# Kernel tuning notes

Measured on AMD Instinct MI355X. Metric: run time of the kernel, lower is better.

The kernel has to match this reference:

```python
import jax, jax.numpy as jnp
import numpy as np

N_NODES = 50000
IN_CH = 128
HID = 128
N_EDGES = 800000


def _glorot(key, shape):
    fan_in, fan_out = shape[0], shape[1]
    lim = (6.0 / (fan_in + fan_out)) ** 0.5
    return jax.random.uniform(key, shape, jnp.float32, -lim, lim)


def setup_inputs() -> dict:
    key = jax.random.key(0)
    ks = jax.random.split(key, 8)
    x = jax.random.normal(ks[0], (N_NODES, IN_CH), jnp.float32)
    edge_index = jax.random.randint(ks[1], (2, N_EDGES), 0, N_NODES, jnp.int64)
    return {
        "x": x,
        "edge_index": edge_index,
        # SAGEConv1: lin_l (with bias) applied to mean-aggregated neighbors,
        # lin_r (no bias) applied to root features (PyG defaults, mean aggr)
        "W1l": _glorot(ks[2], (IN_CH, HID)),
        "b1l": jnp.zeros((HID,), jnp.float32),
        "W1r": _glorot(ks[3], (IN_CH, HID)),
        # SAGEConv2
        "W2l": _glorot(ks[4], (HID, HID)),
        "b2l": jnp.zeros((HID,), jnp.float32),
        "W2r": _glorot(ks[5], (HID, HID)),
        # final Linear(hidden, 1)
        "Wout": _glorot(ks[6], (HID, 1)),
        "bout": jnp.zeros((1,), jnp.float32),
    }


def _sage_conv(x, src, dst, Wl, bl, Wr, n_nodes):
    # gather source features along edges, mean-reduce into destinations
    msgs = x[src]                                                # [E, D]
    sums = jax.ops.segment_sum(msgs, dst, num_segments=n_nodes)  # [N, D]
    cnt = jax.ops.segment_sum(jnp.ones((src.shape[0], 1), x.dtype), dst,
                              num_segments=n_nodes)              # [N, 1]
    agg = sums / jnp.maximum(cnt, 1.0)
    return agg @ Wl + bl + x @ Wr


def reference(x, edge_index, W1l, b1l, W1r, W2l, b2l, W2r, Wout, bout):
    src, dst = edge_index[0], edge_index[1]
    n = x.shape[0]
    h = jax.nn.relu(_sage_conv(x, src, dst, W1l, b1l, W1r, n))
    h = jax.nn.relu(_sage_conv(h, src, dst, W2l, b2l, W2r, n))
    return (h @ Wout + bout).squeeze(-1)  # [N]
```

## Files before the change

### kernel.cpp

```cpp
#include <hip/hip_runtime.h>

#define D 128
#define LSTR 132

typedef __attribute__((ext_vector_type(8))) short short8;
typedef __attribute__((ext_vector_type(4))) float f32x4;

static __device__ __forceinline__ unsigned short f2bf(float f) {
    unsigned u = __float_as_uint(f);
    return (unsigned short)((u + 0x7fffu + ((u >> 16) & 1u)) >> 16);
}
static __device__ __forceinline__ float b2f(unsigned short u) {
    return __uint_as_float(((unsigned)u) << 16);
}


__global__ void prep_kernel(const float* __restrict__ x,
                            const float* __restrict__ W1l,
                            const float* __restrict__ W1r,
                            const float* __restrict__ W2l,
                            const float* __restrict__ W2r,
                            unsigned* __restrict__ xb2,
                            unsigned short* __restrict__ Bt1,
                            unsigned short* __restrict__ Bt2,
                            int* __restrict__ cnt, int NX2, int Ncnt) {
    const int i = blockIdx.x * blockDim.x + threadIdx.x;
    if (i < NX2) {
        const float2 v = *(const float2*)(x + 2 * (size_t)i);
        xb2[i] = (unsigned)f2bf(v.x) | ((unsigned)f2bf(v.y) << 16);
    } else if (i < NX2 + 2 * 32768) {
        const int j = i - NX2;
        const int which = j >> 15;
        const int jj = j & 32767;
        const int n = jj >> 8;
        const int k = jj & 255;
        const float* Wl = which ? W2l : W1l;
        const float* Wr = which ? W2r : W1r;
        const float w = (k < 128) ? Wl[k * 128 + n] : Wr[(k - 128) * 128 + n];
        (which ? Bt2 : Bt1)[jj] = f2bf(w);
    } else if (i < NX2 + 2 * 32768 + Ncnt) {
        cnt[i - NX2 - 2 * 32768] = 0;
    }
}

__global__ void hist_kernel(const int* __restrict__ dst, int E,
                            int* __restrict__ cnt) {
    int i = blockIdx.x * blockDim.x + threadIdx.x;
    if (i < E) atomicAdd(&cnt[dst[i]], 1);
}

__global__ __launch_bounds__(256) void alloc_kernel(
    const int* __restrict__ cnt, int* __restrict__ cursor,
    int* __restrict__ blk_range, int* __restrict__ gctr, int nchunks) {
    const int c = blockIdx.x * 8 + (threadIdx.x >> 5);
    const int l = threadIdx.x & 31;
    if (c >= nchunks) return;
    const int r0 = c * 32;
    const int v = cnt[r0 + l];
    int s = v;
#pragma unroll
    for (int off = 1; off < 32; off <<= 1) {
        const int u = __shfl_up(s, off, 32);
        if (l >= off) s += u;
    }
    const int tot = __shfl(s, 31, 32);
    int base = 0;
    if (l == 0) base = atomicAdd(gctr, tot);
    base = __shfl(base, 0, 32);
    cursor[r0 + l] = base + s - v;
    if (l == 0) {
        blk_range[2 * c] = base;
        blk_range[2 * c + 1] = base + tot;
    }
}

__global__ void fill_kernel(const int* __restrict__ src,
                            const int* __restrict__ dst, int E,
                            int* __restrict__ cursor,
                            unsigned* __restrict__ csr) {
    int e = blockIdx.x * blockDim.x + threadIdx.x;
    if (e < E) {
        int d = dst[e];
        int p = atomicAdd(&cursor[d], 1);
        csr[p] = (unsigned)src[e] | ((unsigned)d << 16);
    }
}

template <bool HEAD>
__global__ __launch_bounds__(256) void sage_kernel(
    const unsigned short* __restrict__ xb, const unsigned* __restrict__ csr,
    const int* __restrict__ cnt, const int* __restrict__ blk_range,
    const unsigned short* __restrict__ Bt,
    const float* __restrict__ bl, const float* __restrict__ Wout,
    const float* __restrict__ bout, unsigned short* __restrict__ hb_out,
    float* __restrict__ out, int N) {
    __shared__ float aggL[32 * LSTR];
    __shared__ float invL[32];
    __shared__ float redH[32 * 2];

    const int b = blockIdx.x;
    const int i0 = b * 32;
    const int t = threadIdx.x;
    const int g = t >> 5;
    const int l = t & 31;
    const int c4 = l << 2;

    for (int i = t; i < 32 * LSTR; i += 256) aggL[i] = 0.f;
    if (t < 32) invL[t] = 1.0f / fmaxf((float)cnt[i0 + t], 1.0f);
    __syncthreads();

    const int rs0 = blk_range[2 * b];
    const int re0 = blk_range[2 * b + 1];
    const int nE = re0 - rs0;
    int e = rs0 + ((nE * g) >> 3);
    const int ee = rs0 + ((nE * (g + 1)) >> 3);

    float4 acc = make_float4(0.f, 0.f, 0.f, 0.f);
    int cur = (e < ee) ? (int)(csr[e] >> 16) - i0 : -1;

    auto load4 = [&](unsigned p) -> float4 {
        const ushort4 u =
            *(const ushort4*)(xb + (size_t)(p & 0xffffu) * D + c4);
        float4 v;
        v.x = b2f(u.x); v.y = b2f(u.y); v.z = b2f(u.z); v.w = b2f(u.w);
        return v;
    };
    auto step = [&](unsigned p, const float4& v) {
        const int r = (int)(p >> 16) - i0;
        if (r != cur) {
            float* q = aggL + cur * LSTR + c4;
            atomicAdd(q + 0, acc.x);
            atomicAdd(q + 1, acc.y);
            atomicAdd(q + 2, acc.z);
            atomicAdd(q + 3, acc.w);
            acc = make_float4(0.f, 0.f, 0.f, 0.f);
            cur = r;
        }
        acc.x += v.x; acc.y += v.y; acc.z += v.z; acc.w += v.w;
    };

    while (e + 8 <= ee) {
        const unsigned p0 = csr[e + 0], p1 = csr[e + 1];
        const unsigned p2 = csr[e + 2], p3 = csr[e + 3];
        const unsigned p4 = csr[e + 4], p5 = csr[e + 5];
        const unsigned p6 = csr[e + 6], p7 = csr[e + 7];
        const float4 v0 = load4(p0), v1 = load4(p1), v2 = load4(p2),
                     v3 = load4(p3), v4 = load4(p4), v5 = load4(p5),
                     v6 = load4(p6), v7 = load4(p7);
        step(p0, v0); step(p1, v1); step(p2, v2); step(p3, v3);
        step(p4, v4); step(p5, v5); step(p6, v6); step(p7, v7);
        e += 8;
    }
    while (e < ee) {
        const unsigned p = csr[e];
        step(p, load4(p));
        ++e;
    }
    if (cur >= 0) {
        float* q = aggL + cur * LSTR + c4;
        atomicAdd(q + 0, acc.x);
        atomicAdd(q + 1, acc.y);
        atomicAdd(q + 2, acc.z);
        atomicAdd(q + 3, acc.w);
    }
    __syncthreads();

    const int wave = t >> 6;
    const int lane = t & 63;
    const int ln = lane & 15;
    const int quad = lane >> 4;
    const int mtile = wave & 1;
    const int nt0 = (wave >> 1) * 4;
    const int mrow = mtile * 16 + ln;
    const int gmr = i0 + mrow;
    const float inv = invL[mrow];

    f32x4 acc4[4] = {f32x4{0.f, 0.f, 0.f, 0.f}, f32x4{0.f, 0.f, 0.f, 0.f},
                     f32x4{0.f, 0.f, 0.f, 0.f}, f32x4{0.f, 0.f, 0.f, 0.f}};

#pragma unroll
    for (int s = 0; s < 4; ++s) {
        const int kb = s * 32 + quad * 8;
        const float* ap = aggL + mrow * LSTR + kb;
        const float4 fa = *(const float4*)ap;
        const float4 fb = *(const float4*)(ap + 4);
        const short8 aA = {(short)f2bf(fa.x * inv), (short)f2bf(fa.y * inv),
                           (short)f2bf(fa.z * inv), (short)f2bf(fa.w * inv),
                           (short)f2bf(fb.x * inv), (short)f2bf(fb.y * inv),
                           (short)f2bf(fb.z * inv), (short)f2bf(fb.w * inv)};
        short8 aX = {0, 0, 0, 0, 0, 0, 0, 0};
        if (gmr < N) aX = *(const short8*)(xb + (size_t)gmr * D + kb);
#pragma unroll
        for (int nt = 0; nt < 4; ++nt) {
            const int n = (nt0 + nt) * 16 + ln;
            const short8 b1 = *(const short8*)(Bt + n * 256 + kb);
            const short8 b2 = *(const short8*)(Bt + n * 256 + 128 + kb);
            acc4[nt] = __builtin_amdgcn_mfma_f32_16x16x32_bf16(aA, b1, acc4[nt],
                                                               0, 0, 0);
            acc4[nt] = __builtin_amdgcn_mfma_f32_16x16x32_bf16(aX, b2, acc4[nt],
                                                               0, 0, 0);
        }
    }

    float biasv[4], woutv[4];
#pragma unroll
    for (int nt = 0; nt < 4; ++nt) {
        const int col = (nt0 + nt) * 16 + ln;
        biasv[nt] = bl[col];
        if (HEAD) woutv[nt] = Wout[col];
    }

    if (!HEAD) {
#pragma unroll
        for (int r = 0; r < 4; ++r) {
            const int gr = i0 + mtile * 16 + quad * 4 + r;
            if (gr < N) {
#pragma unroll
                for (int nt = 0; nt < 4; ++nt) {
                    const int col = (nt0 + nt) * 16 + ln;
                    const float v = fmaxf(acc4[nt][r] + biasv[nt], 0.f);
                    hb_out[(size_t)gr * D + col] = f2bf(v);
                }
            }
        }
    } else {
        const float b0 = bout[0];
#pragma unroll
        for (int r = 0; r < 4; ++r) {
            const int row = mtile * 16 + quad * 4 + r;
            float p = 0.f;
#pragma unroll
            for (int nt = 0; nt < 4; ++nt) {
                const float v = fmaxf(acc4[nt][r] + biasv[nt], 0.f);
                p += v * woutv[nt];
            }
            p += __shfl_xor(p, 1);
            p += __shfl_xor(p, 2);
            p += __shfl_xor(p, 4);
            p += __shfl_xor(p, 8);
            if (ln == 0) redH[row * 2 + (wave >> 1)] = p;
        }
        __syncthreads();
        if (t < 32) {
            const int gr = i0 + t;
            if (gr < N) out[gr] = redH[t * 2] + redH[t * 2 + 1] + b0;
        }
    }
}

extern "C" void kernel_launch(void* const* d_in, const int* in_sizes, int n_in,
                              void* d_out, int out_size, void* d_ws,
                              size_t ws_size, hipStream_t stream) {
    const float* x = (const float*)d_in[0];
    const int* ei = (const int*)d_in[1];
    const float* W1l = (const float*)d_in[2];
    const float* b1l = (const float*)d_in[3];
    const float* W1r = (const float*)d_in[4];
    const float* W2l = (const float*)d_in[5];
    const float* b2l = (const float*)d_in[6];
    const float* W2r = (const float*)d_in[7];
    const float* Wout = (const float*)d_in[8];
    const float* bout = (const float*)d_in[9];

    const int N = in_sizes[0] / D;
    const int E = in_sizes[1] / 2;
    const int* src = ei;
    const int* dst = ei + E;

    const size_t Npad = (size_t)((N + 66 + 255) & ~255);
    const size_t Epad = (size_t)((E + 255) & ~255);
    int* cnt = (int*)d_ws;
    int* gctr = cnt + Npad - 1;
    int* cursor = cnt + Npad;
    int* blk_range = cursor + Npad;
    unsigned* csr = (unsigned*)(blk_range + 4096);
    unsigned short* xb = (unsigned short*)(csr + Epad);
    unsigned short* hb = xb + (size_t)N * D;
    unsigned short* Bt1 = hb + (size_t)N * D;
    unsigned short* Bt2 = Bt1 + 128 * 256;
    float* out = (float*)d_out;

    const int nchunks = (N + 31) / 32;
    const int NX2 = N * D / 2;
    const int prep_total = NX2 + 2 * 32768 + (int)Npad;

    prep_kernel<<<(prep_total + 255) / 256, 256, 0, stream>>>(
        x, W1l, W1r, W2l, W2r, (unsigned*)xb, Bt1, Bt2, cnt, NX2, (int)Npad);
    hist_kernel<<<(E + 255) / 256, 256, 0, stream>>>(dst, E, cnt);
    alloc_kernel<<<(nchunks + 7) / 8, 256, 0, stream>>>(cnt, cursor, blk_range,
                                                        gctr, nchunks);
    fill_kernel<<<(E + 255) / 256, 256, 0, stream>>>(src, dst, E, cursor, csr);

    sage_kernel<false><<<nchunks, 256, 0, stream>>>(
        xb, csr, cnt, blk_range, Bt1, b1l, nullptr, nullptr, hb, nullptr, N);
    sage_kernel<true><<<nchunks, 256, 0, stream>>>(
        hb, csr, cnt, blk_range, Bt2, b2l, Wout, bout, nullptr, out, N);
}
```

Baseline: 313.9 us.

## Replace global-atomic CSR build with block-local tile binning and in-kernel row sort

Replaces the global histogram/alloc/fill CSR construction, which relies on per-node global atomics, with a two-level scheme. Edges are binned per 32-node tile using shared-memory histograms, a per-bin column scan and a single-block prefix scan, then scattered into tile-grouped order. Each sage kernel then counts rows and sorts its tile's edges by destination row in shared memory, falling back to unsorted global reads above a capacity cap. This aims to cut contention from global atomics, but adds more kernel launches, a serial scan over all histogram blocks per bin, and a per-layer in-kernel sort that repeats the same work in both layers.

```diff
diff --git a/kernel.cpp b/kernel.cpp
--- a/kernel.cpp
+++ b/kernel.cpp
@@ -2,6 +2,7 @@
 
 #define D 128
 #define LSTR 132
+#define CAP 3072
 
 typedef __attribute__((ext_vector_type(8))) short short8;
 typedef __attribute__((ext_vector_type(4))) float f32x4;
@@ -22,8 +23,7 @@
                             const float* __restrict__ W2r,
                             unsigned* __restrict__ xb2,
                             unsigned short* __restrict__ Bt1,
-                            unsigned short* __restrict__ Bt2,
-                            int* __restrict__ cnt, int NX2, int Ncnt) {
+                            unsigned short* __restrict__ Bt2, int NX2) {
     const int i = blockIdx.x * blockDim.x + threadIdx.x;
     if (i < NX2) {
         const float2 v = *(const float2*)(x + 2 * (size_t)i);
@@ -38,65 +38,101 @@
         const float* Wr = which ? W2r : W1r;
         const float w = (k < 128) ? Wl[k * 128 + n] : Wr[(k - 128) * 128 + n];
         (which ? Bt2 : Bt1)[jj] = f2bf(w);
-    } else if (i < NX2 + 2 * 32768 + Ncnt) {
-        cnt[i - NX2 - 2 * 32768] = 0;
-    }
-}
-
-__global__ void hist_kernel(const int* __restrict__ dst, int E,
-                            int* __restrict__ cnt) {
-    int i = blockIdx.x * blockDim.x + threadIdx.x;
-    if (i < E) atomicAdd(&cnt[dst[i]], 1);
-}
-
-__global__ __launch_bounds__(256) void alloc_kernel(
-    const int* __restrict__ cnt, int* __restrict__ cursor,
-    int* __restrict__ blk_range, int* __restrict__ gctr, int nchunks) {
-    const int c = blockIdx.x * 8 + (threadIdx.x >> 5);
-    const int l = threadIdx.x & 31;
-    if (c >= nchunks) return;
-    const int r0 = c * 32;
-    const int v = cnt[r0 + l];
-    int s = v;
-#pragma unroll
-    for (int off = 1; off < 32; off <<= 1) {
-        const int u = __shfl_up(s, off, 32);
-        if (l >= off) s += u;
-    }
-    const int tot = __shfl(s, 31, 32);
-    int base = 0;
-    if (l == 0) base = atomicAdd(gctr, tot);
-    base = __shfl(base, 0, 32);
-    cursor[r0 + l] = base + s - v;
-    if (l == 0) {
-        blk_range[2 * c] = base;
-        blk_range[2 * c + 1] = base + tot;
-    }
-}
-
-__global__ void fill_kernel(const int* __restrict__ src,
-                            const int* __restrict__ dst, int E,
-                            int* __restrict__ cursor,
-                            unsigned* __restrict__ csr) {
-    int e = blockIdx.x * blockDim.x + threadIdx.x;
-    if (e < E) {
-        int d = dst[e];
-        int p = atomicAdd(&cursor[d], 1);
-        csr[p] = (unsigned)src[e] | ((unsigned)d << 16);
+    }
+}
+
+__global__ __launch_bounds__(256) void histA_kernel(const int* __restrict__ dst,
+                                                    int E, int nbins,
+                                                    unsigned* __restrict__ G) {
+    __shared__ int h[2048];
+    const int t = threadIdx.x;
+    for (int i = t; i < nbins; i += 256) h[i] = 0;
+    __syncthreads();
+    const int base = blockIdx.x * 1024;
+    for (int i = t; i < 1024; i += 256) {
+        const int e = base + i;
+        if (e < E) atomicAdd(&h[dst[e] >> 5], 1);
+    }
+    __syncthreads();
+    unsigned* g = G + (size_t)blockIdx.x * nbins;
+    for (int i = t; i < nbins; i += 256) g[i] = (unsigned)h[i];
+}
+
+__global__ void scanB_kernel(unsigned* __restrict__ G, int nblkA, int nbins,
+                             int* __restrict__ tot) {
+    const int bin = blockIdx.x * 256 + threadIdx.x;
+    if (bin >= nbins) return;
+    unsigned run = 0;
+    for (int b = 0; b < nblkA; ++b) {
+        unsigned* p = G + (size_t)b * nbins + bin;
+        const unsigned v = *p;
+        *p = run;
+        run += v;
+    }
+    tot[bin] = (int)run;
+}
+
+__global__ __launch_bounds__(1024) void scanC_kernel(
+    const int* __restrict__ tot, int nbins, int* __restrict__ tile_base) {
+    __shared__ int part[1024];
+    const int t = threadIdx.x;
+    const int chunk = (nbins + 1023) >> 10;
+    const int lo = min(t * chunk, nbins);
+    const int hi = min(lo + chunk, nbins);
+    int s = 0;
+    for (int i = lo; i < hi; ++i) s += tot[i];
+    part[t] = s;
+    __syncthreads();
+    for (int off = 1; off < 1024; off <<= 1) {
+        int add = (t >= off) ? part[t - off] : 0;
+        __syncthreads();
+        part[t] += add;
+        __syncthreads();
+    }
+    int excl = (t == 0) ? 0 : part[t - 1];
+    for (int i = lo; i < hi; ++i) {
+        tile_base[i] = excl;
+        excl += tot[i];
+    }
+    if (t == 1023) tile_base[nbins] = part[1023];
+}
+
+__global__ __launch_bounds__(256) void fillB_kernel(
+    const int* __restrict__ src, const int* __restrict__ dst, int E,
+    const unsigned* __restrict__ G, const int* __restrict__ tile_base,
+    unsigned* __restrict__ csr, int nbins) {
+    __shared__ int rank[2048];
+    const int t = threadIdx.x;
+    for (int i = t; i < nbins; i += 256) rank[i] = 0;
+    __syncthreads();
+    const int base = blockIdx.x * 1024;
+    const unsigned* g = G + (size_t)blockIdx.x * nbins;
+    for (int i = t; i < 1024; i += 256) {
+        const int e = base + i;
+        if (e < E) {
+            const int d = dst[e];
+            const int bin = d >> 5;
+            const int r = atomicAdd(&rank[bin], 1);
+            const int pos = tile_base[bin] + (int)g[bin] + r;
+            csr[pos] = (unsigned)src[e] | ((unsigned)d << 16);
+        }
     }
 }
 
 template <bool HEAD>
 __global__ __launch_bounds__(256) void sage_kernel(
     const unsigned short* __restrict__ xb, const unsigned* __restrict__ csr,
-    const int* __restrict__ cnt, const int* __restrict__ blk_range,
+    const int* __restrict__ tile_base,
     const unsigned short* __restrict__ Bt,
     const float* __restrict__ bl, const float* __restrict__ Wout,
     const float* __restrict__ bout, unsigned short* __restrict__ hb_out,
     float* __restrict__ out, int N) {
     __shared__ float aggL[32 * LSTR];
+    __shared__ unsigned sortedE[CAP];
+    __shared__ int rowcnt[32];
+    __shared__ int rowofs[32];
     __shared__ float invL[32];
-    __shared__ float redH[32 * 2];
+    __shared__ float redH[64];
 
     const int b = blockIdx.x;
     const int i0 = b * 32;
@@ -105,18 +141,50 @@
     const int l = t & 31;
     const int c4 = l << 2;
 
+    const int rs0 = tile_base[b];
+    const int re0 = tile_base[b + 1];
+    const int nE = re0 - rs0;
+    const bool use_sorted = (nE <= CAP);
+
     for (int i = t; i < 32 * LSTR; i += 256) aggL[i] = 0.f;
-    if (t < 32) invL[t] = 1.0f / fmaxf((float)cnt[i0 + t], 1.0f);
-    __syncthreads();
-
-    const int rs0 = blk_range[2 * b];
-    const int re0 = blk_range[2 * b + 1];
-    const int nE = re0 - rs0;
-    int e = rs0 + ((nE * g) >> 3);
-    const int ee = rs0 + ((nE * (g + 1)) >> 3);
+    if (t < 32) rowcnt[t] = 0;
+    __syncthreads();
+
+    for (int i = t; i < nE; i += 256)
+        atomicAdd(&rowcnt[(csr[rs0 + i] >> 16) & 31], 1);
+    __syncthreads();
+
+    if (t < 32) {
+        const int v = rowcnt[t];
+        invL[t] = 1.0f / fmaxf((float)v, 1.0f);
+        int s = v;
+#pragma unroll
+        for (int off = 1; off < 32; off <<= 1) {
+            const int u = __shfl_up(s, off, 32);
+            if (l >= off) s += u;
+        }
+        rowofs[t] = s - v;
+    }
+    __syncthreads();
+
+    if (use_sorted) {
+        for (int i = t; i < nE; i += 256) {
+            const unsigned p = csr[rs0 + i];
+            const int k = atomicAdd(&rowofs[(p >> 16) & 31], 1);
+            sortedE[k] = p;
+        }
+    }
+    __syncthreads();
+
+    int e = (nE * g) >> 3;
+    const int ee = (nE * (g + 1)) >> 3;
+
+    auto getp = [&](int idx) -> unsigned {
+        return use_sorted ? sortedE[idx] : csr[rs0 + idx];
+    };
 
     float4 acc = make_float4(0.f, 0.f, 0.f, 0.f);
-    int cur = (e < ee) ? (int)(csr[e] >> 16) - i0 : -1;
+    int cur = (e < ee) ? (int)(getp(e) >> 16) - i0 : -1;
 
     auto load4 = [&](unsigned p) -> float4 {
         const ushort4 u =
@@ -140,10 +208,10 @@
     };
 
     while (e + 8 <= ee) {
-        const unsigned p0 = csr[e + 0], p1 = csr[e + 1];
-        const unsigned p2 = csr[e + 2], p3 = csr[e + 3];
-        const unsigned p4 = csr[e + 4], p5 = csr[e + 5];
-        const unsigned p6 = csr[e + 6], p7 = csr[e + 7];
+        const unsigned p0 = getp(e + 0), p1 = getp(e + 1);
+        const unsigned p2 = getp(e + 2), p3 = getp(e + 3);
+        const unsigned p4 = getp(e + 4), p5 = getp(e + 5);
+        const unsigned p6 = getp(e + 6), p7 = getp(e + 7);
         const float4 v0 = load4(p0), v1 = load4(p1), v2 = load4(p2),
                      v3 = load4(p3), v4 = load4(p4), v5 = load4(p5),
                      v6 = load4(p6), v7 = load4(p7);
@@ -152,7 +220,7 @@
         e += 8;
     }
     while (e < ee) {
-        const unsigned p = csr[e];
+        const unsigned p = getp(e);
         step(p, load4(p));
         ++e;
     }
@@ -267,32 +335,33 @@
     const int* src = ei;
     const int* dst = ei + E;
 
-    const size_t Npad = (size_t)((N + 66 + 255) & ~255);
+    const int nbins = (N + 31) / 32;
+    const int nblkA = (E + 1023) / 1024;
     const size_t Epad = (size_t)((E + 255) & ~255);
-    int* cnt = (int*)d_ws;
-    int* gctr = cnt + Npad - 1;
-    int* cursor = cnt + Npad;
-    int* blk_range = cursor + Npad;
-    unsigned* csr = (unsigned*)(blk_range + 4096);
+
+    int* tot = (int*)d_ws;
+    int* tile_base = tot + 2048;
+    unsigned* G = (unsigned*)(tile_base + 2049 + 3);
+    unsigned* csr = G + (size_t)nblkA * nbins;
     unsigned short* xb = (unsigned short*)(csr + Epad);
     unsigned short* hb = xb + (size_t)N * D;
     unsigned short* Bt1 = hb + (size_t)N * D;
     unsigned short* Bt2 = Bt1 + 128 * 256;
     float* out = (float*)d_out;
 
-    const int nchunks = (N + 31) / 32;
     const int NX2 = N * D / 2;
-    const int prep_total = NX2 + 2 * 32768 + (int)Npad;
+    const int prep_total = NX2 + 2 * 32768;
 
     prep_kernel<<<(prep_total + 255) / 256, 256, 0, stream>>>(
-        x, W1l, W1r, W2l, W2r, (unsigned*)xb, Bt1, Bt2, cnt, NX2, (int)Npad);
-    hist_kernel<<<(E + 255) / 256, 256, 0, stream>>>(dst, E, cnt);
-    alloc_kernel<<<(nchunks + 7) / 8, 256, 0, stream>>>(cnt, cursor, blk_range,
-                                                        gctr, nchunks);
-    fill_kernel<<<(E + 255) / 256, 256, 0, stream>>>(src, dst, E, cursor, csr);
-
-    sage_kernel<false><<<nchunks, 256, 0, stream>>>(
-        xb, csr, cnt, blk_range, Bt1, b1l, nullptr, nullptr, hb, nullptr, N);
-    sage_kernel<true><<<nchunks, 256, 0, stream>>>(
-        hb, csr, cnt, blk_range, Bt2, b2l, Wout, bout, nullptr, out, N);
-}
+        x, W1l, W1r, W2l, W2r, (unsigned*)xb, Bt1, Bt2, NX2);
+    histA_kernel<<<nblkA, 256, 0, stream>>>(dst, E, nbins, G);
+    scanB_kernel<<<(nbins + 255) / 256, 256, 0, stream>>>(G, nblkA, nbins, tot);
+    scanC_kernel<<<1, 1024, 0, stream>>>(tot, nbins, tile_base);
+    fillB_kernel<<<nblkA, 256, 0, stream>>>(src, dst, E, G, tile_base, csr,
+                                            nbins);
+
+    sage_kernel<false><<<nbins, 256, 0, stream>>>(
+        xb, csr, tile_base, Bt1, b1l, nullptr, nullptr, hb, nullptr, N);
+    sage_kernel<true><<<nbins, 256, 0, stream>>>(
+        hb, csr, tile_base, Bt2, b2l, Wout, bout, nullptr, out, N);
+}
```

After: 446.6 us. +42.2%, slower.
